# Kernel optimization log

Measured on AMD Instinct MI355X. Metric: run time of the kernel, lower is better.

Reference implementation:

```python
import jax, jax.numpy as jnp
import numpy as np

N_NODES = 100000
N_EDGES = 1600000
D_IN = 128
CH = [128, 128]
N_GRAPHS = 256


def _glorot(key, shape):
    lim = float(np.sqrt(6.0 / (shape[0] + shape[1])))
    return jax.random.uniform(key, shape, jnp.float32, -lim, lim)


def setup_inputs() -> dict:
    key = jax.random.key(0)
    ks = jax.random.split(key, 12)
    x = jax.random.normal(ks[0], (N_NODES, D_IN), jnp.float32)
    edge_index = jax.random.randint(ks[1], (2, N_EDGES), 0, N_NODES, jnp.int64)
    batch = jnp.sort(jax.random.randint(ks[2], (N_NODES,), 0, N_GRAPHS, jnp.int64))
    W1 = _glorot(ks[3], (D_IN, CH[0]))
    b1 = jnp.zeros((CH[0],), jnp.float32)
    W2 = _glorot(ks[4], (CH[0], CH[1]))
    b2 = jnp.zeros((CH[1],), jnp.float32)
    Wm1 = _glorot(ks[5], (CH[1], 500)); bm1 = jnp.zeros((500,), jnp.float32)
    Wm2 = _glorot(ks[6], (500, 100));   bm2 = jnp.zeros((100,), jnp.float32)
    Wm3 = _glorot(ks[7], (100, 1));     bm3 = jnp.zeros((1,), jnp.float32)
    return {"x": x, "edge_index": edge_index, "batch": batch,
            "W1": W1, "b1": b1, "W2": W2, "b2": b2,
            "Wm1": Wm1, "bm1": bm1, "Wm2": Wm2, "bm2": bm2,
            "Wm3": Wm3, "bm3": bm3}


def gcn_conv(x, W, b, src, dst, n_nodes):
    # GCNConv with add_self_loops=True, symmetric normalization.
    h = x @ W  # [N, C]
    deg = jnp.zeros((n_nodes,), h.dtype).at[dst].add(1.0) + 1.0  # +1 self loop
    dinv = jax.lax.rsqrt(deg)  # deg >= 1
    norm = dinv[src] * dinv[dst]  # [E]
    agg = jnp.zeros_like(h).at[dst].add(h[src] * norm[:, None])
    agg = agg + h * (dinv * dinv)[:, None]  # self-loop term, norm = dinv[i]^2
    return agg + b


def global_mean_pool(x, batch, n_graphs):
    s = jax.ops.segment_sum(x, batch, num_segments=n_graphs)
    cnt = jax.ops.segment_sum(jnp.ones((x.shape[0],), x.dtype), batch, num_segments=n_graphs)
    return s / jnp.maximum(cnt, 1.0)[:, None]


def reference(x, edge_index, batch, W1, b1, W2, b2, Wm1, bm1, Wm2, bm2, Wm3, bm3):
    src, dst = edge_index[0], edge_index[1]
    h = jax.nn.relu(gcn_conv(x, W1, b1, src, dst, N_NODES))
    h = jax.nn.relu(gcn_conv(h, W2, b2, src, dst, N_NODES))
    g = global_mean_pool(h, batch, N_GRAPHS)  # [G, CH1]
    g = jax.nn.relu(g @ Wm1 + bm1)
    g = jax.nn.relu(g @ Wm2 + bm2)
    return g @ Wm3 + bm3  # [G, 1]
```

## Files before the change

kernel.cpp:

```cpp
#include <hip/hip_runtime.h>

#define CDIM 128
#define NGRAPH 256
#define BSH 7
#define BCAP 4096
#define NBLK 256
#define PCHUNK 512

typedef unsigned short bf16_t;
typedef __attribute__((ext_vector_type(8))) short bf16x8;
typedef __attribute__((ext_vector_type(4))) float f32x4;

__device__ __forceinline__ float bflo(unsigned u) { return __uint_as_float(u << 16); }
__device__ __forceinline__ float bfhi(unsigned u) { return __uint_as_float(u & 0xffff0000u); }
__device__ __forceinline__ unsigned short f2bf(float f) {
  unsigned u = __float_as_uint(f);
  u += 0x7fffu + ((u >> 16) & 1u);
  return (unsigned short)(u >> 16);
}

__global__ __launch_bounds__(256) void k_wprep(const float* __restrict__ W1,
    const float* __restrict__ W2, bf16_t* __restrict__ Wtg1, bf16_t* __restrict__ Wtg2) {
  int i = blockIdx.x * 256 + threadIdx.x;
  int n = i >> 7, k = i & 127;
  Wtg1[n * 128 + k] = f2bf(W1[k * 128 + n]);
  Wtg2[n * 128 + k] = f2bf(W2[k * 128 + n]);
}

__global__ __launch_bounds__(1024) void k_phist(const int* __restrict__ dst,
    int* __restrict__ phist, int E, int NB) {
  __shared__ int hist[1024];
  int t = blockIdx.x, tid = threadIdx.x;
  for (int i = tid; i < NB; i += 1024) hist[i] = 0;
  __syncthreads();
  int tile = (E + NBLK - 1) / NBLK;
  int lo = t * tile;
  int hi = lo + tile; if (hi > E) hi = E;
  for (int i = lo + tid; i < hi; i += 1024) atomicAdd(&hist[dst[i] >> BSH], 1);
  __syncthreads();
  for (int i = tid; i < NB; i += 1024) phist[i * NBLK + t] = hist[i];
}

__global__ __launch_bounds__(256) void k_bscan(int* __restrict__ phist,
    int* __restrict__ btot) {
  __shared__ int wsum[4];
  int b = blockIdx.x;
  int tid = threadIdx.x, lane = tid & 63, wave = tid >> 6;
  int orig = phist[b * NBLK + tid];
  int v = orig;
#pragma unroll
  for (int ofs = 1; ofs < 64; ofs <<= 1) {
    int u = __shfl_up(v, ofs, 64);
    if (lane >= ofs) v += u;
  }
  if (lane == 63) wsum[wave] = v;
  __syncthreads();
  int add = 0;
#pragma unroll
  for (int w = 0; w < 3; w++) if (w < wave) add += wsum[w];
  int incl = v + add;
  phist[b * NBLK + tid] = incl - orig;
  if (tid == 255) btot[b] = incl;
}

__global__ __launch_bounds__(1024) void k_boff(const int* __restrict__ bsums,
    int* __restrict__ boffs, int G) {
  __shared__ int sh[1024];
  int tid = threadIdx.x;
  int v = (tid < G) ? bsums[tid] : 0;
  sh[tid] = v;
  __syncthreads();
  for (int ofs = 1; ofs < 1024; ofs <<= 1) {
    int u = (tid >= ofs) ? sh[tid - ofs] : 0;
    __syncthreads();
    sh[tid] += u;
    __syncthreads();
  }
  if (tid < G) boffs[tid] = sh[tid] - v;
  if (tid == G) boffs[G] = (G > 0) ? sh[G - 1] : 0;
}

__global__ __launch_bounds__(1024) void k_pscatter(const int* __restrict__ src,
    const int* __restrict__ dst, const int* __restrict__ phist,
    const int* __restrict__ bbase, unsigned* __restrict__ tmp, int E, int NB) {
  __shared__ int cur[1024];
  int t = blockIdx.x, tid = threadIdx.x;
  for (int i = tid; i < NB; i += 1024) cur[i] = bbase[i] + phist[i * NBLK + t];
  __syncthreads();
  int tile = (E + NBLK - 1) / NBLK;
  int lo = t * tile;
  int hi = lo + tile; if (hi > E) hi = E;
  for (int i = lo + tid; i < hi; i += 1024) {
    int d = dst[i];
    int p = atomicAdd(&cur[d >> BSH], 1);
    tmp[p] = (unsigned)src[i] | ((unsigned)(d & 127) << 20);
  }
}

__global__ __launch_bounds__(256) void k_csort2(const unsigned* __restrict__ tmp,
    const int* __restrict__ bbase, int* __restrict__ rowptr, float* __restrict__ dinv,
    int* __restrict__ col, int N, int NB, int E) {
  __shared__ int hist[128];
  __shared__ int sc[128];
  __shared__ int lcur[128];
  __shared__ unsigned buf[BCAP];
  int b = blockIdx.x;
  int n0 = b << BSH;
  int base = bbase[b];
  int cnt = bbase[b + 1] - base;
  int tid = threadIdx.x;
  if (tid < 128) hist[tid] = 0;
  __syncthreads();
  for (int i = tid; i < cnt; i += 256) atomicAdd(&hist[(tmp[base + i] >> 20) & 127], 1);
  __syncthreads();
  if (tid < 128) sc[tid] = hist[tid];
  __syncthreads();
  for (int ofs = 1; ofs < 128; ofs <<= 1) {
    int v = (tid < 128 && tid >= ofs) ? sc[tid - ofs] : 0;
    __syncthreads();
    if (tid < 128) sc[tid] += v;
    __syncthreads();
  }
  if (tid < 128) {
    int excl = sc[tid] - hist[tid];
    lcur[tid] = excl;
    int node = n0 + tid;
    if (node < N) {
      rowptr[node] = base + excl;
      dinv[node] = rsqrtf((float)hist[tid] + 1.0f);
    }
  }
  if (b == 0 && tid == 0) rowptr[N] = E;
  __syncthreads();
  if (cnt <= BCAP) {
    for (int i = tid; i < cnt; i += 256) {
      unsigned pk = tmp[base + i];
      int p = atomicAdd(&lcur[(pk >> 20) & 127], 1);
      buf[p] = pk & 0xFFFFFu;
    }
    __syncthreads();
    for (int i = tid; i < cnt; i += 256) col[base + i] = (int)buf[i];
  } else {
    for (int i = tid; i < cnt; i += 256) {
      unsigned pk = tmp[base + i];
      int p = atomicAdd(&lcur[(pk >> 20) & 127], 1);
      col[base + p] = (int)(pk & 0xFFFFFu);
    }
  }
}

#define WSTRIDE 136
template <int BF16IN>
__global__ __launch_bounds__(256) void k_gemm(const void* __restrict__ Ap,
    const bf16_t* __restrict__ Wtg, bf16_t* __restrict__ Co, int M) {
  __shared__ bf16_t Wt[128 * WSTRIDE];
  int tid = threadIdx.x;
  for (int c2 = tid; c2 < 2048; c2 += 256) {
    int n = c2 >> 4;
    int k8 = (c2 & 15) << 3;
    *(uint4*)&Wt[n * WSTRIDE + k8] = *(const uint4*)&Wtg[n * 128 + k8];
  }
  __syncthreads();

  int wave = tid >> 6;
  int lane = tid & 63;
  int m = lane & 15;
  int q = lane >> 4;
  int nstrips = (M + 63) >> 6;

  for (int s = blockIdx.x; s < nstrips; s += gridDim.x) {
    int rowA = s * 64 + wave * 16 + m;
    if (rowA > M - 1) rowA = M - 1;
    bf16x8 a[4];
#pragma unroll
    for (int c = 0; c < 4; c++) {
      if (BF16IN) {
        a[c] = *(const bf16x8*)((const bf16_t*)Ap + (size_t)rowA * CDIM + c * 32 + q * 8);
      } else {
        const float* ap = (const float*)Ap + (size_t)rowA * CDIM + c * 32 + q * 8;
        float4 f0 = *(const float4*)ap;
        float4 f1 = *(const float4*)(ap + 4);
        union { bf16x8 v; unsigned short u[8]; } ua;
        ua.u[0] = f2bf(f0.x); ua.u[1] = f2bf(f0.y); ua.u[2] = f2bf(f0.z); ua.u[3] = f2bf(f0.w);
        ua.u[4] = f2bf(f1.x); ua.u[5] = f2bf(f1.y); ua.u[6] = f2bf(f1.z); ua.u[7] = f2bf(f1.w);
        a[c] = ua.v;
      }
    }
#pragma unroll
    for (int t = 0; t < 8; t++) {
      f32x4 acc = {0.f, 0.f, 0.f, 0.f};
#pragma unroll
      for (int c = 0; c < 4; c++) {
        bf16x8 bv = *(const bf16x8*)&Wt[(t * 16 + m) * WSTRIDE + c * 32 + q * 8];
        acc = __builtin_amdgcn_mfma_f32_16x16x32_bf16(a[c], bv, acc, 0, 0, 0);
      }
#pragma unroll
      for (int r = 0; r < 4; r++) {
        int row = s * 64 + wave * 16 + q * 4 + r;
        if (row < M) Co[(size_t)row * CDIM + t * 16 + m] = f2bf(acc[r]);
      }
    }
  }
}

__global__ __launch_bounds__(256) void k_agg(const bf16_t* __restrict__ t,
    const int* __restrict__ rowptr, const int* __restrict__ col,
    const float* __restrict__ dinv, const float* __restrict__ bias,
    bf16_t* __restrict__ out, int N) {
  int wave = threadIdx.x >> 6;
  int lane = threadIdx.x & 63;
  int node = blockIdx.x * 4 + wave;
  if (node >= N) return;
  int half = lane >> 5;
  int c = lane & 31;
  const uint2* tp = (const uint2*)t;
  float di = dinv[node];
  uint2 sv = tp[(size_t)node * 32 + c];
  float sw = (half == 0) ? di : 0.f;
  float a0 = bflo(sv.x) * sw, a1 = bfhi(sv.x) * sw;
  float a2 = bflo(sv.y) * sw, a3 = bfhi(sv.y) * sw;
  int beg = rowptr[node], end = rowptr[node + 1];
  for (int base = beg; base < end; base += 64) {
    int rem = end - base;
    int cnt = rem < 64 ? rem : 64;
    int sL = 0; float wL = 0.f;
    if (lane < cnt) { sL = col[base + lane]; wL = dinv[sL]; }
    for (int k = 0; k < cnt; k += 8) {
      int j0 = k + half, j1 = k + 2 + half, j2 = k + 4 + half, j3 = k + 6 + half;
      int s0 = __shfl(sL, j0, 64); float w0 = __shfl(wL, j0, 64);
      int s1 = __shfl(sL, j1, 64); float w1 = __shfl(wL, j1, 64);
      int s2 = __shfl(sL, j2, 64); float w2 = __shfl(wL, j2, 64);
      int s3 = __shfl(sL, j3, 64); float w3 = __shfl(wL, j3, 64);
      if (j0 >= cnt) { s0 = node; w0 = 0.f; }
      if (j1 >= cnt) { s1 = node; w1 = 0.f; }
      if (j2 >= cnt) { s2 = node; w2 = 0.f; }
      if (j3 >= cnt) { s3 = node; w3 = 0.f; }
      uint2 v0 = tp[(size_t)s0 * 32 + c];
      uint2 v1 = tp[(size_t)s1 * 32 + c];
      uint2 v2 = tp[(size_t)s2 * 32 + c];
      uint2 v3 = tp[(size_t)s3 * 32 + c];
      a0 = fmaf(bflo(v0.x), w0, a0); a1 = fmaf(bfhi(v0.x), w0, a1);
      a2 = fmaf(bflo(v0.y), w0, a2); a3 = fmaf(bfhi(v0.y), w0, a3);
      a0 = fmaf(bflo(v1.x), w1, a0); a1 = fmaf(bfhi(v1.x), w1, a1);
      a2 = fmaf(bflo(v1.y), w1, a2); a3 = fmaf(bfhi(v1.y), w1, a3);
      a0 = fmaf(bflo(v2.x), w2, a0); a1 = fmaf(bfhi(v2.x), w2, a1);
      a2 = fmaf(bflo(v2.y), w2, a2); a3 = fmaf(bfhi(v2.y), w2, a3);
      a0 = fmaf(bflo(v3.x), w3, a0); a1 = fmaf(bfhi(v3.x), w3, a1);
      a2 = fmaf(bflo(v3.y), w3, a2); a3 = fmaf(bfhi(v3.y), w3, a3);
    }
  }
  a0 += __shfl_xor(a0, 32, 64);
  a1 += __shfl_xor(a1, 32, 64);
  a2 += __shfl_xor(a2, 32, 64);
  a3 += __shfl_xor(a3, 32, 64);
  if (half == 0) {
    float4 bb = ((const float4*)bias)[c];
    float o0 = fmaxf(fmaf(di, a0, bb.x), 0.f);
    float o1 = fmaxf(fmaf(di, a1, bb.y), 0.f);
    float o2 = fmaxf(fmaf(di, a2, bb.z), 0.f);
    float o3 = fmaxf(fmaf(di, a3, bb.w), 0.f);
    uint2 o;
    o.x = ((unsigned)f2bf(o1) << 16) | f2bf(o0);
    o.y = ((unsigned)f2bf(o3) << 16) | f2bf(o2);
    ((uint2*)(out + (size_t)node * CDIM))[c] = o;
  }
}

__global__ __launch_bounds__(256) void k_pool2(const bf16_t* __restrict__ h,
    const int* __restrict__ batch, float* __restrict__ gsum, int N) {
  int tid = threadIdx.x;
  int wave = tid >> 6, lane = tid & 63;
  int i0 = blockIdx.x * PCHUNK;
  int i1 = i0 + PCHUNK; if (i1 > N) i1 = N;
  float ax = 0.f, ay = 0.f;
  int curb = -1;
  for (int i = i0 + wave; i < i1; i += 4) {
    int b = batch[i];
    if (b != curb) {
      if (curb >= 0) {
        atomicAdd(&gsum[curb * CDIM + lane * 2], ax);
        atomicAdd(&gsum[curb * CDIM + lane * 2 + 1], ay);
      }
      curb = b; ax = 0.f; ay = 0.f;
    }
    unsigned u = ((const unsigned*)(h + (size_t)i * CDIM))[lane];
    ax += bflo(u); ay += bfhi(u);
  }
  if (curb >= 0) {
    atomicAdd(&gsum[curb * CDIM + lane * 2], ax);
    atomicAdd(&gsum[curb * CDIM + lane * 2 + 1], ay);
  }
}

__global__ __launch_bounds__(512) void k_mlp1(const float* __restrict__ g,
    const int* __restrict__ batch, int N,
    const float* __restrict__ W, const float* __restrict__ b, float* __restrict__ o) {
  __shared__ float gs[CDIM];
  int bi = blockIdx.x, tid = threadIdx.x;
  if (tid < CDIM) {
    int lo = 0, hi = N;
    while (lo < hi) { int mid = (lo + hi) >> 1; if (batch[mid] < bi) lo = mid + 1; else hi = mid; }
    int s = lo;
    lo = 0; hi = N;
    int key = bi + 1;
    while (lo < hi) { int mid = (lo + hi) >> 1; if (batch[mid] < key) lo = mid + 1; else hi = mid; }
    float inv = 1.f / fmaxf((float)(lo - s), 1.f);
    gs[tid] = g[bi * CDIM + tid] * inv;
  }
  __syncthreads();
  if (tid < 500) {
    float acc = b[tid];
#pragma unroll 4
    for (int k = 0; k < CDIM; k++) acc = fmaf(gs[k], W[k * 500 + tid], acc);
    o[bi * 500 + tid] = fmaxf(acc, 0.f);
  }
}

__global__ __launch_bounds__(128) void k_mlp2(const float* __restrict__ a,
    const float* __restrict__ W, const float* __restrict__ b, float* __restrict__ o) {
  __shared__ float as[500];
  int bi = blockIdx.x, tid = threadIdx.x;
  for (int k = tid; k < 500; k += 128) as[k] = a[bi * 500 + k];
  __syncthreads();
  if (tid < 100) {
    float acc = b[tid];
    for (int k = 0; k < 500; k++) acc = fmaf(as[k], W[k * 100 + tid], acc);
    o[bi * 100 + tid] = fmaxf(acc, 0.f);
  }
}

__global__ __launch_bounds__(64) void k_mlp3(const float* __restrict__ a,
    const float* __restrict__ w, const float* __restrict__ b, float* __restrict__ o) {
  int bi = blockIdx.x, lane = threadIdx.x;
  float v = a[bi * 100 + lane] * w[lane];
  if (lane + 64 < 100) v = fmaf(a[bi * 100 + lane + 64], w[lane + 64], v);
#pragma unroll
  for (int ofs = 32; ofs > 0; ofs >>= 1) v += __shfl_down(v, ofs, 64);
  if (lane == 0) o[bi] = v + b[0];
}

static inline size_t align_up(size_t v) { return (v + 255) & ~(size_t)255; }

extern "C" void kernel_launch(void* const* d_in, const int* in_sizes, int n_in,
                              void* d_out, int out_size, void* d_ws, size_t ws_size,
                              hipStream_t stream) {
  const float* x   = (const float*)d_in[0];
  const int*   ei  = (const int*)d_in[1];
  const int*   bat = (const int*)d_in[2];
  const float* W1  = (const float*)d_in[3];
  const float* b1  = (const float*)d_in[4];
  const float* W2  = (const float*)d_in[5];
  const float* b2  = (const float*)d_in[6];
  const float* Wm1 = (const float*)d_in[7];
  const float* bm1 = (const float*)d_in[8];
  const float* Wm2 = (const float*)d_in[9];
  const float* bm2 = (const float*)d_in[10];
  const float* Wm3 = (const float*)d_in[11];
  const float* bm3 = (const float*)d_in[12];
  float* out = (float*)d_out;

  const int E = in_sizes[1] / 2;
  const int N = in_sizes[2];
  const int* src = ei;
  const int* dst = ei + E;
  const int NB = (N + 127) >> BSH;
  const int M  = NB * NBLK;

  char* p = (char*)d_ws;
  bf16_t* t    = (bf16_t*)p;   p += align_up((size_t)N * CDIM * 2);
  bf16_t* h    = (bf16_t*)p;   p += align_up((size_t)N * CDIM * 2);
  int* rowptr  = (int*)p;      p += align_up((size_t)(N + 1) * 4);
  int* colx    = (int*)p;      p += align_up((size_t)E * 4);
  unsigned* tmp= (unsigned*)p; p += align_up((size_t)E * 4);
  float* dinv  = (float*)p;    p += align_up((size_t)N * 4);
  int* phist   = (int*)p;      p += align_up((size_t)M * 4);
  int* btot    = (int*)p;      p += align_up((size_t)NB * 4);
  int* bbase   = (int*)p;      p += align_up((size_t)(NB + 1) * 4);
  bf16_t* Wtg1 = (bf16_t*)p;   p += align_up((size_t)CDIM * CDIM * 2);
  bf16_t* Wtg2 = (bf16_t*)p;   p += align_up((size_t)CDIM * CDIM * 2);
  float* gb    = (float*)p;    p += align_up((size_t)NGRAPH * CDIM * 4);
  float* m1    = (float*)p;    p += align_up((size_t)NGRAPH * 500 * 4);
  float* m2    = (float*)p;    p += align_up((size_t)NGRAPH * 100 * 4);
  (void)ws_size; (void)n_in; (void)out_size;

  hipMemsetAsync(gb, 0, (size_t)NGRAPH * CDIM * 4, stream);

  k_wprep<<<64, 256, 0, stream>>>(W1, W2, Wtg1, Wtg2);
  k_phist<<<NBLK, 1024, 0, stream>>>(dst, phist, E, NB);
  k_bscan<<<NB, 256, 0, stream>>>(phist, btot);
  k_boff<<<1, 1024, 0, stream>>>(btot, bbase, NB);
  k_pscatter<<<NBLK, 1024, 0, stream>>>(src, dst, phist, bbase, tmp, E, NB);
  k_csort2<<<NB, 256, 0, stream>>>(tmp, bbase, rowptr, dinv, colx, N, NB, E);

  k_gemm<0><<<512, 256, 0, stream>>>(x, Wtg1, t, N);
  k_agg<<<(N + 3) / 4, 256, 0, stream>>>(t, rowptr, colx, dinv, b1, h, N);
  k_gemm<1><<<512, 256, 0, stream>>>(h, Wtg2, t, N);
  k_agg<<<(N + 3) / 4, 256, 0, stream>>>(t, rowptr, colx, dinv, b2, h, N);

  k_pool2<<<(N + PCHUNK - 1) / PCHUNK, 256, 0, stream>>>(h, bat, gb, N);
  k_mlp1<<<NGRAPH, 512, 0, stream>>>(gb, bat, N, Wm1, bm1, m1);
  k_mlp2<<<NGRAPH, 128, 0, stream>>>(m1, Wm2, bm2, m2);
  k_mlp3<<<NGRAPH, 64, 0, stream>>>(m2, Wm3, bm3, out);
}
```

Before: 378.6 us.

## Fuse mean-pool into second aggregation and merge final MLP layers

The second GCN aggregation now accumulates per-graph sums directly, with each wave handling 16 consecutive nodes and flushing atomics when the batch id changes. This removes the write and re-read of the second hidden layer and drops the separate pooling kernel. The gather loop is also widened to 8 outstanding neighbor loads per iteration, and the last two MLP layers are merged into one kernel. In exchange, the pooled aggregation launches 16x fewer waves and runs each wave serially over its nodes, which lowers parallelism and latency hiding for the irregular gather.

```diff
diff --git a/kernel.cpp b/kernel.cpp
--- a/kernel.cpp
+++ b/kernel.cpp
@@ -5,7 +5,6 @@
 #define BSH 7
 #define BCAP 4096
 #define NBLK 256
-#define PCHUNK 512
 
 typedef unsigned short bf16_t;
 typedef __attribute__((ext_vector_type(8))) short bf16x8;
@@ -203,92 +202,91 @@
   }
 }
 
+template <int POOL>
 __global__ __launch_bounds__(256) void k_agg(const bf16_t* __restrict__ t,
     const int* __restrict__ rowptr, const int* __restrict__ col,
     const float* __restrict__ dinv, const float* __restrict__ bias,
-    bf16_t* __restrict__ out, int N) {
+    bf16_t* __restrict__ out, const int* __restrict__ batch,
+    float* __restrict__ gsum, int N) {
   int wave = threadIdx.x >> 6;
   int lane = threadIdx.x & 63;
-  int node = blockIdx.x * 4 + wave;
-  if (node >= N) return;
   int half = lane >> 5;
   int c = lane & 31;
   const uint2* tp = (const uint2*)t;
-  float di = dinv[node];
-  uint2 sv = tp[(size_t)node * 32 + c];
-  float sw = (half == 0) ? di : 0.f;
-  float a0 = bflo(sv.x) * sw, a1 = bfhi(sv.x) * sw;
-  float a2 = bflo(sv.y) * sw, a3 = bfhi(sv.y) * sw;
-  int beg = rowptr[node], end = rowptr[node + 1];
-  for (int base = beg; base < end; base += 64) {
-    int rem = end - base;
-    int cnt = rem < 64 ? rem : 64;
-    int sL = 0; float wL = 0.f;
-    if (lane < cnt) { sL = col[base + lane]; wL = dinv[sL]; }
-    for (int k = 0; k < cnt; k += 8) {
-      int j0 = k + half, j1 = k + 2 + half, j2 = k + 4 + half, j3 = k + 6 + half;
-      int s0 = __shfl(sL, j0, 64); float w0 = __shfl(wL, j0, 64);
-      int s1 = __shfl(sL, j1, 64); float w1 = __shfl(wL, j1, 64);
-      int s2 = __shfl(sL, j2, 64); float w2 = __shfl(wL, j2, 64);
-      int s3 = __shfl(sL, j3, 64); float w3 = __shfl(wL, j3, 64);
-      if (j0 >= cnt) { s0 = node; w0 = 0.f; }
-      if (j1 >= cnt) { s1 = node; w1 = 0.f; }
-      if (j2 >= cnt) { s2 = node; w2 = 0.f; }
-      if (j3 >= cnt) { s3 = node; w3 = 0.f; }
-      uint2 v0 = tp[(size_t)s0 * 32 + c];
-      uint2 v1 = tp[(size_t)s1 * 32 + c];
-      uint2 v2 = tp[(size_t)s2 * 32 + c];
-      uint2 v3 = tp[(size_t)s3 * 32 + c];
-      a0 = fmaf(bflo(v0.x), w0, a0); a1 = fmaf(bfhi(v0.x), w0, a1);
-      a2 = fmaf(bflo(v0.y), w0, a2); a3 = fmaf(bfhi(v0.y), w0, a3);
-      a0 = fmaf(bflo(v1.x), w1, a0); a1 = fmaf(bfhi(v1.x), w1, a1);
-      a2 = fmaf(bflo(v1.y), w1, a2); a3 = fmaf(bfhi(v1.y), w1, a3);
-      a0 = fmaf(bflo(v2.x), w2, a0); a1 = fmaf(bfhi(v2.x), w2, a1);
-      a2 = fmaf(bflo(v2.y), w2, a2); a3 = fmaf(bfhi(v2.y), w2, a3);
-      a0 = fmaf(bflo(v3.x), w3, a0); a1 = fmaf(bfhi(v3.x), w3, a1);
-      a2 = fmaf(bflo(v3.y), w3, a2); a3 = fmaf(bfhi(v3.y), w3, a3);
-    }
-  }
-  a0 += __shfl_xor(a0, 32, 64);
-  a1 += __shfl_xor(a1, 32, 64);
-  a2 += __shfl_xor(a2, 32, 64);
-  a3 += __shfl_xor(a3, 32, 64);
-  if (half == 0) {
-    float4 bb = ((const float4*)bias)[c];
-    float o0 = fmaxf(fmaf(di, a0, bb.x), 0.f);
-    float o1 = fmaxf(fmaf(di, a1, bb.y), 0.f);
-    float o2 = fmaxf(fmaf(di, a2, bb.z), 0.f);
-    float o3 = fmaxf(fmaf(di, a3, bb.w), 0.f);
-    uint2 o;
-    o.x = ((unsigned)f2bf(o1) << 16) | f2bf(o0);
-    o.y = ((unsigned)f2bf(o3) << 16) | f2bf(o2);
-    ((uint2*)(out + (size_t)node * CDIM))[c] = o;
-  }
-}
-
-__global__ __launch_bounds__(256) void k_pool2(const bf16_t* __restrict__ h,
-    const int* __restrict__ batch, float* __restrict__ gsum, int N) {
-  int tid = threadIdx.x;
-  int wave = tid >> 6, lane = tid & 63;
-  int i0 = blockIdx.x * PCHUNK;
-  int i1 = i0 + PCHUNK; if (i1 > N) i1 = N;
-  float ax = 0.f, ay = 0.f;
-  int curb = -1;
-  for (int i = i0 + wave; i < i1; i += 4) {
-    int b = batch[i];
-    if (b != curb) {
-      if (curb >= 0) {
-        atomicAdd(&gsum[curb * CDIM + lane * 2], ax);
-        atomicAdd(&gsum[curb * CDIM + lane * 2 + 1], ay);
+  float4 bb = ((const float4*)bias)[c];
+  int n0, nEnd;
+  if (POOL) { n0 = (blockIdx.x * 4 + wave) * 16; nEnd = n0 + 16; }
+  else      { n0 = blockIdx.x * 4 + wave;        nEnd = n0 + 1; }
+  if (n0 >= N) return;
+  if (nEnd > N) nEnd = N;
+  float p0 = 0.f, p1 = 0.f, p2 = 0.f, p3 = 0.f;
+  int curb = POOL ? batch[n0] : 0;
+
+  for (int node = n0; node < nEnd; node++) {
+    float di = dinv[node];
+    uint2 sv = tp[(size_t)node * 32 + c];
+    float sw = (half == 0) ? di : 0.f;
+    float a0 = bflo(sv.x) * sw, a1 = bfhi(sv.x) * sw;
+    float a2 = bflo(sv.y) * sw, a3 = bfhi(sv.y) * sw;
+    int beg = rowptr[node], end = rowptr[node + 1];
+    for (int base = beg; base < end; base += 64) {
+      int rem = end - base;
+      int cnt = rem < 64 ? rem : 64;
+      int sL = 0; float wL = 0.f;
+      if (lane < cnt) { sL = col[base + lane]; wL = dinv[sL]; }
+      for (int k = 0; k < cnt; k += 16) {
+        int s[8]; float w[8];
+#pragma unroll
+        for (int i = 0; i < 8; i++) {
+          int j = k + 2 * i + half;
+          s[i] = __shfl(sL, j, 64); w[i] = __shfl(wL, j, 64);
+          if (j >= cnt) { s[i] = node; w[i] = 0.f; }
+        }
+        uint2 v[8];
+#pragma unroll
+        for (int i = 0; i < 8; i++) v[i] = tp[(size_t)s[i] * 32 + c];
+#pragma unroll
+        for (int i = 0; i < 8; i++) {
+          a0 = fmaf(bflo(v[i].x), w[i], a0); a1 = fmaf(bfhi(v[i].x), w[i], a1);
+          a2 = fmaf(bflo(v[i].y), w[i], a2); a3 = fmaf(bfhi(v[i].y), w[i], a3);
+        }
       }
-      curb = b; ax = 0.f; ay = 0.f;
-    }
-    unsigned u = ((const unsigned*)(h + (size_t)i * CDIM))[lane];
-    ax += bflo(u); ay += bfhi(u);
-  }
-  if (curb >= 0) {
-    atomicAdd(&gsum[curb * CDIM + lane * 2], ax);
-    atomicAdd(&gsum[curb * CDIM + lane * 2 + 1], ay);
+    }
+    a0 += __shfl_xor(a0, 32, 64);
+    a1 += __shfl_xor(a1, 32, 64);
+    a2 += __shfl_xor(a2, 32, 64);
+    a3 += __shfl_xor(a3, 32, 64);
+    if (half == 0) {
+      float o0 = fmaxf(fmaf(di, a0, bb.x), 0.f);
+      float o1 = fmaxf(fmaf(di, a1, bb.y), 0.f);
+      float o2 = fmaxf(fmaf(di, a2, bb.z), 0.f);
+      float o3 = fmaxf(fmaf(di, a3, bb.w), 0.f);
+      if (!POOL) {
+        uint2 o;
+        o.x = ((unsigned)f2bf(o1) << 16) | f2bf(o0);
+        o.y = ((unsigned)f2bf(o3) << 16) | f2bf(o2);
+        ((uint2*)(out + (size_t)node * CDIM))[c] = o;
+      } else {
+        int b = batch[node];
+        if (b != curb) {
+          atomicAdd(&gsum[curb * CDIM + c * 4 + 0], p0);
+          atomicAdd(&gsum[curb * CDIM + c * 4 + 1], p1);
+          atomicAdd(&gsum[curb * CDIM + c * 4 + 2], p2);
+          atomicAdd(&gsum[curb * CDIM + c * 4 + 3], p3);
+          curb = b; p0 = p1 = p2 = p3 = 0.f;
+        }
+        p0 += __uint_as_float((unsigned)f2bf(o0) << 16);
+        p1 += __uint_as_float((unsigned)f2bf(o1) << 16);
+        p2 += __uint_as_float((unsigned)f2bf(o2) << 16);
+        p3 += __uint_as_float((unsigned)f2bf(o3) << 16);
+      }
+    }
+  }
+  if (POOL && half == 0) {
+    atomicAdd(&gsum[curb * CDIM + c * 4 + 0], p0);
+    atomicAdd(&gsum[curb * CDIM + c * 4 + 1], p1);
+    atomicAdd(&gsum[curb * CDIM + c * 4 + 2], p2);
+    atomicAdd(&gsum[curb * CDIM + c * 4 + 3], p3);
   }
 }
 
@@ -316,27 +314,27 @@
   }
 }
 
-__global__ __launch_bounds__(128) void k_mlp2(const float* __restrict__ a,
-    const float* __restrict__ W, const float* __restrict__ b, float* __restrict__ o) {
+__global__ __launch_bounds__(128) void k_mlp23(const float* __restrict__ a,
+    const float* __restrict__ W2m, const float* __restrict__ b2m,
+    const float* __restrict__ w3, const float* __restrict__ b3,
+    float* __restrict__ o) {
   __shared__ float as[500];
+  __shared__ float m2s[100];
   int bi = blockIdx.x, tid = threadIdx.x;
   for (int k = tid; k < 500; k += 128) as[k] = a[bi * 500 + k];
   __syncthreads();
   if (tid < 100) {
-    float acc = b[tid];
-    for (int k = 0; k < 500; k++) acc = fmaf(as[k], W[k * 100 + tid], acc);
-    o[bi * 100 + tid] = fmaxf(acc, 0.f);
-  }
-}
-
-__global__ __launch_bounds__(64) void k_mlp3(const float* __restrict__ a,
-    const float* __restrict__ w, const float* __restrict__ b, float* __restrict__ o) {
-  int bi = blockIdx.x, lane = threadIdx.x;
-  float v = a[bi * 100 + lane] * w[lane];
-  if (lane + 64 < 100) v = fmaf(a[bi * 100 + lane + 64], w[lane + 64], v);
-#pragma unroll
-  for (int ofs = 32; ofs > 0; ofs >>= 1) v += __shfl_down(v, ofs, 64);
-  if (lane == 0) o[bi] = v + b[0];
+    float acc = b2m[tid];
+    for (int k = 0; k < 500; k++) acc = fmaf(as[k], W2m[k * 100 + tid], acc);
+    m2s[tid] = fmaxf(acc, 0.f) * w3[tid];
+  }
+  __syncthreads();
+  if (tid < 64) {
+    float v = m2s[tid] + ((tid + 64 < 100) ? m2s[tid + 64] : 0.f);
+#pragma unroll
+    for (int ofs = 32; ofs > 0; ofs >>= 1) v += __shfl_down(v, ofs, 64);
+    if (tid == 0) o[bi] = v + b3[0];
+  }
 }
 
 static inline size_t align_up(size_t v) { return (v + 255) & ~(size_t)255; }
@@ -380,7 +378,6 @@
   bf16_t* Wtg2 = (bf16_t*)p;   p += align_up((size_t)CDIM * CDIM * 2);
   float* gb    = (float*)p;    p += align_up((size_t)NGRAPH * CDIM * 4);
   float* m1    = (float*)p;    p += align_up((size_t)NGRAPH * 500 * 4);
-  float* m2    = (float*)p;    p += align_up((size_t)NGRAPH * 100 * 4);
   (void)ws_size; (void)n_in; (void)out_size;
 
   hipMemsetAsync(gb, 0, (size_t)NGRAPH * CDIM * 4, stream);
@@ -393,12 +390,13 @@
   k_csort2<<<NB, 256, 0, stream>>>(tmp, bbase, rowptr, dinv, colx, N, NB, E);
 
   k_gemm<0><<<512, 256, 0, stream>>>(x, Wtg1, t, N);
-  k_agg<<<(N + 3) / 4, 256, 0, stream>>>(t, rowptr, colx, dinv, b1, h, N);
+  k_agg<0><<<(N + 3) / 4, 256, 0, stream>>>(t, rowptr, colx, dinv, b1, h,
+                                            bat, gb, N);
   k_gemm<1><<<512, 256, 0, stream>>>(h, Wtg2, t, N);
-  k_agg<<<(N + 3) / 4, 256, 0, stream>>>(t, rowptr, colx, dinv, b2, h, N);
-
-  k_pool2<<<(N + PCHUNK - 1) / PCHUNK, 256, 0, stream>>>(h, bat, gb, N);
+  int pwaves = (N + 15) / 16;
+  k_agg<1><<<(pwaves + 3) / 4, 256, 0, stream>>>(t, rowptr, colx, dinv, b2,
+                                                 (bf16_t*)nullptr, bat, gb, N);
+
   k_mlp1<<<NGRAPH, 512, 0, stream>>>(gb, bat, N, Wm1, bm1, m1);
-  k_mlp2<<<NGRAPH, 128, 0, stream>>>(m1, Wm2, bm2, m2);
-  k_mlp3<<<NGRAPH, 64, 0, stream>>>(m2, Wm3, bm3, out);
-}
+  k_mlp23<<<NGRAPH, 128, 0, stream>>>(m1, Wm2, bm2, Wm3, bm3, out);
+}
```

After: 360.7 us. 4.7% less time.
